# Performance work log

Hardware: AMD Instinct MI355X
Metric: run time of the kernel (lower is better)

## Reference

```python
import jax, jax.numpy as jnp
import numpy as np

# Dimensions: decode-style paged attention with INT4 + Hamming(8,4) SECDED ECC
B, Q, S, H, KVH, D = 8, 16, 4096, 32, 8, 128
BLOCK_SIZE = 16
BLOCKS_PER_SEQ = S // BLOCK_SIZE      # 256
NUM_BLOCKS = B * BLOCKS_PER_SEQ       # 2048


def _bit(x, i):
    return (x >> i) & 1


def hamming84_encode(nib):
    """Encode 4-bit nibbles (int32 in [0,16)) into Hamming(8,4) SECDED codewords.
    Bit layout (0-indexed): [p1, p2, d1, p4, d2, d3, d4, overall_parity]."""
    d1, d2, d3, d4 = _bit(nib, 0), _bit(nib, 1), _bit(nib, 2), _bit(nib, 3)
    p1 = d1 ^ d2 ^ d4
    p2 = d1 ^ d3 ^ d4
    p4 = d2 ^ d3 ^ d4
    cw7 = p1 | (p2 << 1) | (d1 << 2) | (p4 << 3) | (d2 << 4) | (d3 << 5) | (d4 << 6)
    par = p1 ^ p2 ^ d1 ^ p4 ^ d2 ^ d3 ^ d4
    return cw7 | (par << 7)


def hamming84_decode(cw):
    """Syndrome decode: correct single-bit errors (syndrome!=0, overall parity odd),
    detect-but-pass-through double errors. Returns the 4-bit nibble."""
    b = [_bit(cw, i) for i in range(8)]
    s1 = b[0] ^ b[2] ^ b[4] ^ b[6]
    s2 = b[1] ^ b[2] ^ b[5] ^ b[6]
    s4 = b[3] ^ b[4] ^ b[5] ^ b[6]
    syn = s1 + 2 * s2 + 4 * s4
    overall = b[0] ^ b[1] ^ b[2] ^ b[3] ^ b[4] ^ b[5] ^ b[6] ^ b[7]
    flip = jnp.where((syn > 0) & (overall == 1),
                     jnp.left_shift(jnp.int32(1), jnp.maximum(syn - 1, 0)),
                     jnp.int32(0))
    cwc = cw ^ flip
    return _bit(cwc, 2) | (_bit(cwc, 4) << 1) | (_bit(cwc, 5) << 2) | (_bit(cwc, 6) << 3)


def quantize_int4(x):
    """Symmetric per-token per-head INT4 quant: scale = absmax/7, nibble in [0,16)."""
    scale = jnp.maximum(jnp.max(jnp.abs(x), axis=-1) / 7.0, 1e-8)  # [B,S,KVH]
    nib = jnp.clip(jnp.round(x / scale[..., None]), -8, 7).astype(jnp.int32) + 8
    return nib, scale


def write_and_read(x, block_table):
    """Quantize -> Hamming84 encode -> scatter into paged cache via block table,
    then gather -> decode -> dequantize. x: [B,S,KVH,D] float."""
    nib, scale = quantize_int4(x)
    cw = hamming84_encode(nib)
    bt = block_table.reshape(-1)                                   # [B*BLOCKS_PER_SEQ]
    cw_blocks = cw.reshape(B * BLOCKS_PER_SEQ, BLOCK_SIZE, KVH, D)
    sc_blocks = scale.reshape(B * BLOCKS_PER_SEQ, BLOCK_SIZE, KVH)
    cache = jnp.zeros((NUM_BLOCKS, BLOCK_SIZE, KVH, D), dtype=jnp.int32).at[bt].set(cw_blocks)
    scales = jnp.zeros((NUM_BLOCKS, BLOCK_SIZE, KVH), dtype=x.dtype).at[bt].set(sc_blocks)
    g_cw = cache[bt].reshape(B, S, KVH, D)
    g_sc = scales[bt].reshape(B, S, KVH)
    nib_dec = hamming84_decode(g_cw)
    return (nib_dec.astype(x.dtype) - 8.0) * g_sc[..., None]


def setup_inputs() -> dict:
    key = jax.random.key(0)
    kq, kk, kv = jax.random.split(key, 3)
    q = jax.random.normal(kq, (B, Q, H, D), dtype=jnp.float32)
    k = jax.random.normal(kk, (B, S, KVH, D), dtype=jnp.float32)
    v = jax.random.normal(kv, (B, S, KVH, D), dtype=jnp.float32)
    block_table = jnp.arange(NUM_BLOCKS, dtype=jnp.int32).reshape(B, BLOCKS_PER_SEQ)
    return {"q": q, "k": k, "v": v, "block_table": block_table}


def reference(q, k, v, block_table):
    k_d = write_and_read(k, block_table)   # [B,S,KVH,D] dequantized keys
    v_d = write_and_read(v, block_table)
    G = H // KVH
    qg = q.reshape(B, Q, KVH, G, D)
    scores = jnp.einsum('bqhgd,bshd->bhgqs', qg, k_d) / jnp.sqrt(jnp.float32(D))
    # queries are the last Q positions of the S-token context (causal)
    qpos = S - Q + jnp.arange(Q)
    kpos = jnp.arange(S)
    mask = kpos[None, :] <= qpos[:, None]                          # [Q,S]
    scores = jnp.where(mask[None, None, None], scores, jnp.float32(-1e30))
    attn = jax.nn.softmax(scores, axis=-1)
    out = jnp.einsum('bhgqs,bshd->bqhgd', attn, v_d)
    return out.reshape(B, Q, H, D)
```

## Files before the change

kernel.cpp:

```cpp
#include <hip/hip_runtime.h>
#include <hip/hip_bf16.h>

#define B_    8
#define Qn    16
#define S_    4096
#define Hh    32
#define KVH_  8
#define D_    128
#define G_    4
#define ROWS  64
#define KT    32
#define NT_TOT (S_ / KT)
#define NCHUNK 12
#define THREADS 256
#define VTS   40

typedef unsigned int u32;
typedef unsigned short u16;
typedef __attribute__((ext_vector_type(8))) short short8;
typedef __attribute__((ext_vector_type(4))) float f32x4;

__device__ __forceinline__ u16 f2bf(float f){
  union{float f; u32 u;} t; t.f = f; u32 u = t.u;
  return (u16)((u + 0x7fffu + ((u >> 16) & 1u)) >> 16);
}
__device__ __forceinline__ float bf2f(u16 h){
  union{u32 x; float f;} t; t.x = ((u32)h) << 16; return t.f;
}
__device__ __forceinline__ u16 qnib(float x, float inv){
  union{float f; u32 u;} t; t.f = rintf(x * inv);
  return (u16)(t.u >> 16);
}

__device__ __forceinline__ void gll16(const float* g, const float* lds){
  __builtin_amdgcn_global_load_lds((const __attribute__((address_space(1))) void*)g,
                                   (__attribute__((address_space(3))) void*)lds,
                                   16, 0, 0);
}

__global__ __launch_bounds__(THREADS)
__attribute__((amdgpu_waves_per_eu(3)))
void attn_partial(const float* __restrict__ q, const float* __restrict__ k,
                  const float* __restrict__ v, float* __restrict__ part_o,
                  float* __restrict__ part_ml)
{
  __shared__ float rawK[KT * D_];
  __shared__ float rawV[KT * D_];
  __shared__ u16   kn[KT * D_];
  __shared__ u16   vt[D_ * VTS];
  __shared__ float kscale[KT];
  __shared__ float vscale[KT];

  const int chunk = blockIdx.x;
  const int kvh   = blockIdx.y;
  const int b     = blockIdx.z;
  const int tid   = threadIdx.x;
  const int lane  = tid & 63;
  const int w     = tid >> 6;
  const int l15   = lane & 15;
  const int l4    = lane >> 4;
  const int t0    = (chunk * NT_TOT) / NCHUNK;
  const int t1    = ((chunk + 1) * NT_TOT) / NCHUNK;
  const float RS = 0.08838834764831844f;

  const int lt  = tid >> 3;
  const int qd4 = (tid & 7) * 4;

  short8 qhi[4], qlo[4];
  {
    const int h = kvh * G_ + w;
    const float* qp = q + (((size_t)(b * Qn + l15) * Hh) + h) * (size_t)D_ + (l4 * 8);
    #pragma unroll
    for (int kc = 0; kc < 4; ++kc){
      const float4 a = *(const float4*)(qp + kc * 32);
      const float4 c = *(const float4*)(qp + kc * 32 + 4);
      const float fv[8] = {a.x, a.y, a.z, a.w, c.x, c.y, c.z, c.w};
      #pragma unroll
      for (int i = 0; i < 8; ++i){
        const u16 hi = f2bf(fv[i]);
        qhi[kc][i] = (short)hi;
        qlo[kc][i] = (short)f2bf(fv[i] - bf2f(hi));
      }
    }
  }

  float m_i = -1e30f, l_i = 0.f;
  f32x4 acc_o[8];
  #pragma unroll
  for (int df = 0; df < 8; ++df) acc_o[df] = (f32x4)0.f;

  const int lhi = lane >> 5, cp = lane & 31;
  int goff[4];
  #pragma unroll
  for (int j = 0; j < 4; ++j){
    const int tokp = (w * 4 + j) * 2 + lhi;
    goff[j] = tokp * (KVH_ * D_) + (cp << 2);
  }
  const size_t tb0 = ((size_t)b * S_) * KVH_ * D_ + (size_t)kvh * D_;

  {
    const size_t base = tb0 + (size_t)(t0 * KT) * KVH_ * D_;
    #pragma unroll
    for (int j = 0; j < 4; ++j) gll16(k + base + goff[j], &rawK[(w * 4 + j) * 256]);
    #pragma unroll
    for (int j = 0; j < 4; ++j) gll16(v + base + goff[j], &rawV[(w * 4 + j) * 256]);
  }

  for (int t = t0; t < t1; ++t){
    const int s0 = t * KT;

    asm volatile("s_waitcnt vmcnt(0)" ::: "memory");
    __builtin_amdgcn_sched_barrier(0);
    __builtin_amdgcn_s_barrier();
    __builtin_amdgcn_sched_barrier(0);

    {
      float4 r4[4]; float am = 0.f;
      #pragma unroll
      for (int m = 0; m < 4; ++m){
        r4[m] = *(const float4*)&rawK[lt * D_ + qd4 + m * 32];
        am = fmaxf(am, fmaxf(fmaxf(fabsf(r4[m].x), fabsf(r4[m].y)),
                             fmaxf(fabsf(r4[m].z), fabsf(r4[m].w))));
      }
      am = fmaxf(am, __shfl_xor(am, 1));
      am = fmaxf(am, __shfl_xor(am, 2));
      am = fmaxf(am, __shfl_xor(am, 4));
      const float sc = fmaxf(am * (1.f / 7.f), 1e-8f);
      if ((tid & 7) == 0) kscale[lt] = sc;
      const float inv = 1.f / sc;
      #pragma unroll
      for (int m = 0; m < 4; ++m){
        const int d0 = qd4 + m * 32;
        const int idx = lt * D_ + ((((d0 >> 3) ^ (lt & 7)) << 3) | (d0 & 7));
        *(ushort4*)&kn[idx] = make_ushort4(qnib(r4[m].x, inv), qnib(r4[m].y, inv),
                                           qnib(r4[m].z, inv), qnib(r4[m].w, inv));
      }
    }
    {
      float4 r4[4]; float am = 0.f;
      #pragma unroll
      for (int m = 0; m < 4; ++m){
        r4[m] = *(const float4*)&rawV[lt * D_ + qd4 + m * 32];
        am = fmaxf(am, fmaxf(fmaxf(fabsf(r4[m].x), fabsf(r4[m].y)),
                             fmaxf(fabsf(r4[m].z), fabsf(r4[m].w))));
      }
      am = fmaxf(am, __shfl_xor(am, 1));
      am = fmaxf(am, __shfl_xor(am, 2));
      am = fmaxf(am, __shfl_xor(am, 4));
      const float sc = fmaxf(am * (1.f / 7.f), 1e-8f);
      if ((tid & 7) == 0) vscale[lt] = sc;
      const float inv = 1.f / sc;
      #pragma unroll
      for (int m = 0; m < 4; ++m){
        const int d0 = qd4 + m * 32;
        vt[(d0 + 0) * VTS + lt] = qnib(r4[m].x, inv);
        vt[(d0 + 1) * VTS + lt] = qnib(r4[m].y, inv);
        vt[(d0 + 2) * VTS + lt] = qnib(r4[m].z, inv);
        vt[(d0 + 3) * VTS + lt] = qnib(r4[m].w, inv);
      }
    }
    asm volatile("s_waitcnt lgkmcnt(0)" ::: "memory");
    __builtin_amdgcn_sched_barrier(0);
    __builtin_amdgcn_s_barrier();
    __builtin_amdgcn_sched_barrier(0);

    {
      const int sn = (s0 + KT <= S_ - KT) ? (s0 + KT) : (S_ - KT);
      const size_t base = tb0 + (size_t)sn * KVH_ * D_;
      #pragma unroll
      for (int j = 0; j < 4; ++j) gll16(k + base + goff[j], &rawK[(w * 4 + j) * 256]);
      #pragma unroll
      for (int j = 0; j < 4; ++j) gll16(v + base + goff[j], &rawV[(w * 4 + j) * 256]);
    }

    f32x4 st[2];
    st[0] = (f32x4)0.f; st[1] = (f32x4)0.f;
    __builtin_amdgcn_s_setprio(1);
    #pragma unroll
    for (int kc = 0; kc < 4; ++kc){
      #pragma unroll
      for (int cf = 0; cf < 2; ++cf){
        const int tok = cf * 16 + l15;
        const int gr  = kc * 4 + l4;
        const short8 kf = *(const short8*)&kn[tok * D_ + ((gr ^ (tok & 7)) << 3)];
        st[cf] = __builtin_amdgcn_mfma_f32_16x16x32_bf16(kf, qhi[kc], st[cf], 0, 0, 0);
        st[cf] = __builtin_amdgcn_mfma_f32_16x16x32_bf16(kf, qlo[kc], st[cf], 0, 0, 0);
      }
    }
    __builtin_amdgcn_s_setprio(0);

    float ksr[2][4], vsv[2][4];
    #pragma unroll
    for (int cf = 0; cf < 2; ++cf){
      const float4 ks = *(const float4*)&kscale[cf * 16 + l4 * 4];
      const float4 vs = *(const float4*)&vscale[cf * 16 + l4 * 4];
      ksr[cf][0] = ks.x * RS; ksr[cf][1] = ks.y * RS;
      ksr[cf][2] = ks.z * RS; ksr[cf][3] = ks.w * RS;
      vsv[cf][0] = vs.x; vsv[cf][1] = vs.y; vsv[cf][2] = vs.z; vsv[cf][3] = vs.w;
    }
    const bool need_mask = (s0 + KT > S_ - Qn);
    float x[2][4]; float rm = -1e30f;
    #pragma unroll
    for (int cf = 0; cf < 2; ++cf)
      #pragma unroll
      for (int r = 0; r < 4; ++r){
        float xx = st[cf][r] * ksr[cf][r];
        if (need_mask && (s0 + cf * 16 + l4 * 4 + r > S_ - Qn + l15)) xx = -1e30f;
        x[cf][r] = xx; rm = fmaxf(rm, xx);
      }
    rm = fmaxf(rm, __shfl_xor(rm, 16));
    rm = fmaxf(rm, __shfl_xor(rm, 32));
    const float mn  = fmaxf(m_i, rm);
    const float fac = __expf(m_i - mn);
    m_i = mn;
    float p[2][4]; float rs = 0.f;
    #pragma unroll
    for (int cf = 0; cf < 2; ++cf)
      #pragma unroll
      for (int r = 0; r < 4; ++r){
        p[cf][r] = __expf(x[cf][r] - mn);
        rs += p[cf][r];
      }
    rs += __shfl_xor(rs, 16);
    rs += __shfl_xor(rs, 32);
    l_i = l_i * fac + rs;

    u32 pk0[2], pk1[2];
    #pragma unroll
    for (int rp = 0; rp < 2; ++rp){
      pk0[rp] = (u32)f2bf(p[0][2*rp] * vsv[0][2*rp]) | ((u32)f2bf(p[0][2*rp+1] * vsv[0][2*rp+1]) << 16);
      pk1[rp] = (u32)f2bf(p[1][2*rp] * vsv[1][2*rp]) | ((u32)f2bf(p[1][2*rp+1] * vsv[1][2*rp+1]) << 16);
    }
    const int s0L = ((l4 & 1) * 2) * 16 + l15;
    const int s1L = s0L + 16;
    const u32 a00 = __shfl((int)pk0[0], s0L), a01 = __shfl((int)pk0[1], s0L);
    const u32 a02 = __shfl((int)pk0[0], s1L), a03 = __shfl((int)pk0[1], s1L);
    const u32 a10 = __shfl((int)pk1[0], s0L), a11 = __shfl((int)pk1[1], s0L);
    const u32 a12 = __shfl((int)pk1[0], s1L), a13 = __shfl((int)pk1[1], s1L);
    const bool hi = (l4 >= 2);
    union { uint4 u; short8 s; } pfu;
    pfu.u = make_uint4(hi ? a10 : a00, hi ? a11 : a01,
                       hi ? a12 : a02, hi ? a13 : a03);
    const short8 pf = pfu.s;

    f32x4 facv;
    #pragma unroll
    for (int r = 0; r < 4; ++r) facv[r] = __shfl(fac, l4 * 4 + r);
    #pragma unroll
    for (int df = 0; df < 8; ++df) acc_o[df] *= facv;

    __builtin_amdgcn_s_setprio(1);
    #pragma unroll
    for (int df = 0; df < 8; ++df){
      const int d = df * 16 + l15;
      const short8 vf = *(const short8*)&vt[d * VTS + l4 * 8];
      acc_o[df] = __builtin_amdgcn_mfma_f32_16x16x32_bf16(pf, vf, acc_o[df], 0, 0, 0);
    }
    __builtin_amdgcn_s_setprio(0);
  }

  asm volatile("s_waitcnt vmcnt(0)" ::: "memory");
  __builtin_amdgcn_sched_barrier(0);

  {
    const size_t base = (((size_t)b * KVH_ + kvh) * (size_t)NCHUNK + chunk) * ROWS;
    #pragma unroll
    for (int r = 0; r < 4; ++r){
      const int qrow = (w << 4) + (l4 << 2) + r;
      #pragma unroll
      for (int df = 0; df < 8; ++df)
        part_o[(base + qrow) * D_ + df * 16 + l15] = acc_o[df][r];
    }
    if (l4 == 0){
      part_ml[(base + (w << 4) + l15) * 2 + 0] = m_i;
      part_ml[(base + (w << 4) + l15) * 2 + 1] = l_i;
    }
  }
}

__global__ void attn_reduce(const float* __restrict__ part_o, const float* __restrict__ part_ml,
                            float* __restrict__ out)
{
  const int row = blockIdx.x;
  const int kvh = blockIdx.y;
  const int b   = blockIdx.z;
  const int d   = threadIdx.x;
  const size_t base = ((size_t)b * KVH_ + kvh) * (size_t)NCHUNK;

  float M = -1e30f;
  for (int c = 0; c < NCHUNK; ++c)
    M = fmaxf(M, part_ml[((base + c) * ROWS + row) * 2 + 0]);
  float acc = 0.f, lt = 0.f;
  #pragma unroll
  for (int c = 0; c < NCHUNK; ++c){
    const float m = part_ml[((base + c) * ROWS + row) * 2 + 0];
    const float l = part_ml[((base + c) * ROWS + row) * 2 + 1];
    const float w = __expf(m - M);
    lt += w * l;
    acc += w * part_o[((base + c) * ROWS + row) * D_ + d];
  }
  const int g = row >> 4, qi = row & 15;
  out[(((size_t)b * Qn + qi) * Hh + kvh * G_ + g) * (size_t)D_ + d] = acc / lt;
}

extern "C" void kernel_launch(void* const* d_in, const int* in_sizes, int n_in,
                              void* d_out, int out_size, void* d_ws, size_t ws_size,
                              hipStream_t stream)
{
  const float* q = (const float*)d_in[0];
  const float* k = (const float*)d_in[1];
  const float* v = (const float*)d_in[2];
  float* out = (float*)d_out;

  float* part_o  = (float*)d_ws;
  float* part_ml = part_o + (size_t)B_ * KVH_ * NCHUNK * ROWS * D_;

  attn_partial<<<dim3(NCHUNK, KVH_, B_), THREADS, 0, stream>>>(q, k, v, part_o, part_ml);
  attn_reduce<<<dim3(ROWS, KVH_, B_), 128, 0, stream>>>(part_o, part_ml, out);
}
```

Measured before the change: 64.29 us.

## Double-buffer K/V staging with two-tile-ahead prefetch and fewer chunks

Replaces the single raw K/V LDS buffer with two 32KB buffers that reuse raw space for the quantized kn/vt tiles and scales. Tiles are prefetched two iterations ahead, waiting only on the older tile's loads (vmcnt(8)). The next-tile issue moves to the end of the iteration after a barrier, so global latency can overlap two iterations of compute. NCHUNK drops from 12 to 8 and waves_per_eu from 3 to 2, giving fewer, longer blocks with more LDS each, at the cost of lower occupancy and parallelism.

Measured after the change: 76.77 us. +19.4%, slower.

```diff
diff --git a/kernel.cpp b/kernel.cpp
--- a/kernel.cpp
+++ b/kernel.cpp
@@ -11,7 +11,7 @@
 #define ROWS  64
 #define KT    32
 #define NT_TOT (S_ / KT)
-#define NCHUNK 12
+#define NCHUNK 8
 #define THREADS 256
 #define VTS   40
 
@@ -32,24 +32,19 @@
   return (u16)(t.u >> 16);
 }
 
-__device__ __forceinline__ void gll16(const float* g, const float* lds){
+__device__ __forceinline__ void gll16(const float* g, const void* lds){
   __builtin_amdgcn_global_load_lds((const __attribute__((address_space(1))) void*)g,
                                    (__attribute__((address_space(3))) void*)lds,
                                    16, 0, 0);
 }
 
 __global__ __launch_bounds__(THREADS)
-__attribute__((amdgpu_waves_per_eu(3)))
+__attribute__((amdgpu_waves_per_eu(2)))
 void attn_partial(const float* __restrict__ q, const float* __restrict__ k,
                   const float* __restrict__ v, float* __restrict__ part_o,
                   float* __restrict__ part_ml)
 {
-  __shared__ float rawK[KT * D_];
-  __shared__ float rawV[KT * D_];
-  __shared__ u16   kn[KT * D_];
-  __shared__ u16   vt[D_ * VTS];
-  __shared__ float kscale[KT];
-  __shared__ float vscale[KT];
+  __shared__ __attribute__((aligned(16))) char smem[2][32768];
 
   const int chunk = blockIdx.x;
   const int kvh   = blockIdx.y;
@@ -59,8 +54,8 @@
   const int w     = tid >> 6;
   const int l15   = lane & 15;
   const int l4    = lane >> 4;
-  const int t0    = (chunk * NT_TOT) / NCHUNK;
-  const int t1    = ((chunk + 1) * NT_TOT) / NCHUNK;
+  const int t0    = chunk * (NT_TOT / NCHUNK);
+  const int t1    = t0 + (NT_TOT / NCHUNK);
   const float RS = 0.08838834764831844f;
 
   const int lt  = tid >> 3;
@@ -98,80 +93,86 @@
   }
   const size_t tb0 = ((size_t)b * S_) * KVH_ * D_ + (size_t)kvh * D_;
 
-  {
-    const size_t base = tb0 + (size_t)(t0 * KT) * KVH_ * D_;
-    #pragma unroll
-    for (int j = 0; j < 4; ++j) gll16(k + base + goff[j], &rawK[(w * 4 + j) * 256]);
-    #pragma unroll
-    for (int j = 0; j < 4; ++j) gll16(v + base + goff[j], &rawV[(w * 4 + j) * 256]);
+  #pragma unroll
+  for (int pi = 0; pi < 2; ++pi){
+    const int tp = t0 + pi;
+    const size_t base = tb0 + (size_t)(tp * KT) * KVH_ * D_;
+    char* dst = smem[tp & 1];
+    #pragma unroll
+    for (int j = 0; j < 4; ++j) gll16(k + base + goff[j], dst + (w * 4 + j) * 1024);
+    #pragma unroll
+    for (int j = 0; j < 4; ++j) gll16(v + base + goff[j], dst + 16384 + (w * 4 + j) * 1024);
   }
 
   for (int t = t0; t < t1; ++t){
     const int s0 = t * KT;
-
-    asm volatile("s_waitcnt vmcnt(0)" ::: "memory");
+    char* sm = smem[t & 1];
+    const float* rawK = (const float*)sm;
+    const float* rawV = (const float*)(sm + 16384);
+    u16*   kn  = (u16*)sm;
+    u16*   vt  = (u16*)(sm + 8192);
+    float* ksc = (float*)(sm + 18432);
+    float* vsc = (float*)(sm + 18560);
+
+    asm volatile("s_waitcnt vmcnt(8)" ::: "memory");
+    __builtin_amdgcn_sched_barrier(0);
+
+    float4 kr[4], vr[4];
+    #pragma unroll
+    for (int m = 0; m < 4; ++m){
+      kr[m] = *(const float4*)(rawK + lt * D_ + qd4 + m * 32);
+      vr[m] = *(const float4*)(rawV + lt * D_ + qd4 + m * 32);
+    }
+    asm volatile("s_waitcnt lgkmcnt(0)" ::: "memory");
     __builtin_amdgcn_sched_barrier(0);
     __builtin_amdgcn_s_barrier();
     __builtin_amdgcn_sched_barrier(0);
 
     {
-      float4 r4[4]; float am = 0.f;
-      #pragma unroll
-      for (int m = 0; m < 4; ++m){
-        r4[m] = *(const float4*)&rawK[lt * D_ + qd4 + m * 32];
-        am = fmaxf(am, fmaxf(fmaxf(fabsf(r4[m].x), fabsf(r4[m].y)),
-                             fmaxf(fabsf(r4[m].z), fabsf(r4[m].w))));
-      }
+      float am = 0.f;
+      #pragma unroll
+      for (int m = 0; m < 4; ++m)
+        am = fmaxf(am, fmaxf(fmaxf(fabsf(kr[m].x), fabsf(kr[m].y)),
+                             fmaxf(fabsf(kr[m].z), fabsf(kr[m].w))));
       am = fmaxf(am, __shfl_xor(am, 1));
       am = fmaxf(am, __shfl_xor(am, 2));
       am = fmaxf(am, __shfl_xor(am, 4));
       const float sc = fmaxf(am * (1.f / 7.f), 1e-8f);
-      if ((tid & 7) == 0) kscale[lt] = sc;
+      if ((tid & 7) == 0) ksc[lt] = sc;
       const float inv = 1.f / sc;
       #pragma unroll
       for (int m = 0; m < 4; ++m){
         const int d0 = qd4 + m * 32;
         const int idx = lt * D_ + ((((d0 >> 3) ^ (lt & 7)) << 3) | (d0 & 7));
-        *(ushort4*)&kn[idx] = make_ushort4(qnib(r4[m].x, inv), qnib(r4[m].y, inv),
-                                           qnib(r4[m].z, inv), qnib(r4[m].w, inv));
+        *(ushort4*)&kn[idx] = make_ushort4(qnib(kr[m].x, inv), qnib(kr[m].y, inv),
+                                           qnib(kr[m].z, inv), qnib(kr[m].w, inv));
       }
     }
     {
-      float4 r4[4]; float am = 0.f;
-      #pragma unroll
-      for (int m = 0; m < 4; ++m){
-        r4[m] = *(const float4*)&rawV[lt * D_ + qd4 + m * 32];
-        am = fmaxf(am, fmaxf(fmaxf(fabsf(r4[m].x), fabsf(r4[m].y)),
-                             fmaxf(fabsf(r4[m].z), fabsf(r4[m].w))));
-      }
+      float am = 0.f;
+      #pragma unroll
+      for (int m = 0; m < 4; ++m)
+        am = fmaxf(am, fmaxf(fmaxf(fabsf(vr[m].x), fabsf(vr[m].y)),
+                             fmaxf(fabsf(vr[m].z), fabsf(vr[m].w))));
       am = fmaxf(am, __shfl_xor(am, 1));
       am = fmaxf(am, __shfl_xor(am, 2));
       am = fmaxf(am, __shfl_xor(am, 4));
       const float sc = fmaxf(am * (1.f / 7.f), 1e-8f);
-      if ((tid & 7) == 0) vscale[lt] = sc;
+      if ((tid & 7) == 0) vsc[lt] = sc;
       const float inv = 1.f / sc;
       #pragma unroll
       for (int m = 0; m < 4; ++m){
         const int d0 = qd4 + m * 32;
-        vt[(d0 + 0) * VTS + lt] = qnib(r4[m].x, inv);
-        vt[(d0 + 1) * VTS + lt] = qnib(r4[m].y, inv);
-        vt[(d0 + 2) * VTS + lt] = qnib(r4[m].z, inv);
-        vt[(d0 + 3) * VTS + lt] = qnib(r4[m].w, inv);
+        vt[(d0 + 0) * VTS + lt] = qnib(vr[m].x, inv);
+        vt[(d0 + 1) * VTS + lt] = qnib(vr[m].y, inv);
+        vt[(d0 + 2) * VTS + lt] = qnib(vr[m].z, inv);
+        vt[(d0 + 3) * VTS + lt] = qnib(vr[m].w, inv);
       }
     }
     asm volatile("s_waitcnt lgkmcnt(0)" ::: "memory");
     __builtin_amdgcn_sched_barrier(0);
     __builtin_amdgcn_s_barrier();
     __builtin_amdgcn_sched_barrier(0);
-
-    {
-      const int sn = (s0 + KT <= S_ - KT) ? (s0 + KT) : (S_ - KT);
-      const size_t base = tb0 + (size_t)sn * KVH_ * D_;
-      #pragma unroll
-      for (int j = 0; j < 4; ++j) gll16(k + base + goff[j], &rawK[(w * 4 + j) * 256]);
-      #pragma unroll
-      for (int j = 0; j < 4; ++j) gll16(v + base + goff[j], &rawV[(w * 4 + j) * 256]);
-    }
 
     f32x4 st[2];
     st[0] = (f32x4)0.f; st[1] = (f32x4)0.f;
@@ -192,8 +193,8 @@
     float ksr[2][4], vsv[2][4];
     #pragma unroll
     for (int cf = 0; cf < 2; ++cf){
-      const float4 ks = *(const float4*)&kscale[cf * 16 + l4 * 4];
-      const float4 vs = *(const float4*)&vscale[cf * 16 + l4 * 4];
+      const float4 ks = *(const float4*)&ksc[cf * 16 + l4 * 4];
+      const float4 vs = *(const float4*)&vsc[cf * 16 + l4 * 4];
       ksr[cf][0] = ks.x * RS; ksr[cf][1] = ks.y * RS;
       ksr[cf][2] = ks.z * RS; ksr[cf][3] = ks.w * RS;
       vsv[cf][0] = vs.x; vsv[cf][1] = vs.y; vsv[cf][2] = vs.z; vsv[cf][3] = vs.w;
@@ -257,6 +258,17 @@
       acc_o[df] = __builtin_amdgcn_mfma_f32_16x16x32_bf16(pf, vf, acc_o[df], 0, 0, 0);
     }
     __builtin_amdgcn_s_setprio(0);
+
+    __builtin_amdgcn_s_barrier();
+    __builtin_amdgcn_sched_barrier(0);
+    {
+      const int tn = (t + 2 < NT_TOT) ? t + 2 : NT_TOT - 1;
+      const size_t base = tb0 + (size_t)(tn * KT) * KVH_ * D_;
+      #pragma unroll
+      for (int j = 0; j < 4; ++j) gll16(k + base + goff[j], sm + (w * 4 + j) * 1024);
+      #pragma unroll
+      for (int j = 0; j < 4; ++j) gll16(v + base + goff[j], sm + 16384 + (w * 4 + j) * 1024);
+    }
   }
 
   asm volatile("s_waitcnt vmcnt(0)" ::: "memory");
```
